# Performance work log

Measured on AMD Instinct MI355X. Metric: run time of the kernel, lower is better.

Reference implementation:

```python
import math
import jax, jax.numpy as jnp
import numpy as np

B, T_BI, D_BI = 64, 3000, 128
T_SW, D_SW = 375, 192
T_S1, D_S1 = 188, 192
N_FIRES = 300          # static fire count (target_lengths all = 300 -> beta = 1, ceil(sum)=300)
D_MODEL = 512
SCALE = 4.0            # scale_factor
EPS_LN = 1e-5


def _cif_integrate(h, alpha, thr, n_fires):
    """Vectorized CIF: cumsum + two scatter-adds (matches torch _cif_forward).
    h [B,T,D], alpha [B,T], thr [B,1] -> [B,n_fires,D]."""
    Bq, T, D = h.shape
    a = alpha / thr                       # normalize so boundaries sit at integers
    c = jnp.cumsum(a, axis=1)
    prev = c - a
    kp = jnp.floor(prev)
    kc = jnp.floor(c)
    fired = kc > kp                       # frame crosses a token boundary
    w_hi = jnp.where(fired, (c - kc) * thr, 0.0)          # leftover into new token
    w_lo = jnp.where(fired, (kp + 1.0 - prev) * thr, alpha)  # portion completing old token
    ip = jnp.clip(kp.astype(jnp.int32), 0, n_fires - 1)
    ic = jnp.clip(kc.astype(jnp.int32), 0, n_fires - 1)
    bidx = jnp.broadcast_to(jnp.arange(Bq)[:, None], (Bq, T))
    out = jnp.zeros((Bq, n_fires, D), h.dtype)
    out = out.at[bidx, ip].add(w_lo[..., None] * h)
    out = out.at[bidx, ic].add(w_hi[..., None] * h)
    return out


def _interp(src, t_cont, t_bi):
    """Linear interp of src [B,Ts,D] at continuous fire times t_cont [B,N] (given on the T_bi grid)."""
    Bq, Ts, D = src.shape
    t = t_cont * Ts / t_bi
    lo = jnp.clip(t.astype(jnp.int32), 0, Ts - 2)
    w = (t - lo.astype(t.dtype))[..., None]
    idx_lo = jnp.broadcast_to(lo[..., None], (Bq, t.shape[1], D))
    g_lo = jnp.take_along_axis(src, idx_lo, axis=1)
    g_hi = jnp.take_along_axis(src, idx_lo + 1, axis=1)
    return (1.0 - w) * g_lo + w * g_hi


def _forward(fire_signal, acoustic_src, acoustic_src_s1, conv_w, ln_g, ln_b, wp_w, wp_b,
             film_s0_w, film_s0_b, film_s1_w, film_s1_b, tproj_w, tproj_b,
             aproj_w, aproj_b, bproj_w, bproj_b, target_lengths):
    Bq, T_bi, _ = fire_signal.shape
    # 1) weight predictor: depthwise conv (k=1, no bias) -> LN -> Linear -> sigmoid
    x = fire_signal * conv_w                                   # depthwise 1x1 conv
    mu = jnp.mean(x, axis=-1, keepdims=True)
    var = jnp.var(x, axis=-1, keepdims=True)
    xn = (x - mu) * jax.lax.rsqrt(var + EPS_LN) * ln_g + ln_b
    alpha = SCALE * jax.nn.sigmoid(xn @ wp_w + wp_b)           # [B,T]
    tgt = target_lengths.astype(alpha.dtype)
    qty_loss = jnp.mean(jnp.abs(jnp.sum(alpha, axis=1) - tgt))
    # training-mode alpha normalization (sum alpha_cif == target)
    sum_a = jnp.clip(jnp.sum(alpha, axis=1, keepdims=True), 1e-8)
    alpha_cif = alpha * (tgt[:, None] / sum_a)
    # dynamic threshold beta = sum / ceil(sum)  (== 1 here since targets are integers)
    sum_cif = jnp.sum(alpha_cif, axis=1)
    ceil_sum = jax.lax.stop_gradient(jnp.clip(jnp.ceil(sum_cif), 1.0))
    thr = (sum_cif / ceil_sum)[:, None]                        # [B,1]
    # 2) CIF integration of temporal channel
    acoustic_temporal = _cif_integrate(fire_signal, alpha_cif, thr, N_FIRES)  # [B,N,128]
    # continuous fire times
    cum = jnp.cumsum(alpha_cif, axis=1)
    thresholds = jnp.arange(1, N_FIRES + 1, dtype=alpha.dtype)[None, :] * thr  # [B,N]
    ff = jax.vmap(jnp.searchsorted)(cum, thresholds)
    ff = jnp.minimum(ff, T_bi - 1)
    t_lo = jnp.maximum(ff - 1, 0)
    cum_at = jnp.take_along_axis(cum, t_lo, axis=1)
    a_at = jnp.take_along_axis(alpha_cif, ff, axis=1)
    t_cont = t_lo.astype(alpha.dtype) + (thresholds - cum_at) / jnp.clip(a_at, 1e-8)
    t_cont = jnp.clip(t_cont, 0.0, T_bi - 1)
    # 3) S0 pitch channel: interp + FiLM
    acoustic_pitch = _interp(acoustic_src, t_cont, T_bi)       # [B,N,192]
    film0 = acoustic_temporal @ film_s0_w + film_s0_b
    g0, b0 = jnp.split(film0, 2, axis=-1)
    pitch_mod = g0 * acoustic_pitch + b0
    # 4) project + combine
    embs = (acoustic_temporal @ tproj_w + tproj_b) + (pitch_mod @ aproj_w + aproj_b)
    # S1 beat channel
    acoustic_beat = _interp(acoustic_src_s1, t_cont, T_bi)     # [B,N,192]
    film1 = acoustic_temporal @ film_s1_w + film_s1_b
    g1, b1 = jnp.split(film1, 2, axis=-1)
    beat_mod = g1 * acoustic_beat + b1
    embs = embs + (beat_mod @ bproj_w + bproj_b)
    return embs, alpha, qty_loss


def setup_inputs() -> dict:
    key = jax.random.key(0)
    ks = jax.random.split(key, 14)
    # weight_proj bias init per module: alpha_init = target_fires/encoder_len
    p = min((128.0 / 3000.0) / SCALE, 0.99)
    wp_bias = math.log(p / (1.0 - p))
    f32 = jnp.float32
    return {
        "fire_signal": jax.random.normal(ks[0], (B, T_BI, D_BI), f32),
        "acoustic_src": jax.random.normal(ks[1], (B, T_SW, D_SW), f32),
        "acoustic_src_s1": jax.random.normal(ks[2], (B, T_S1, D_S1), f32),
        "target_lengths": jnp.full((B,), N_FIRES, jnp.int32),
        "conv_w": 1.0 + 0.1 * jax.random.normal(ks[3], (D_BI,), f32),
        "ln_g": jnp.ones((D_BI,), f32),
        "ln_b": jnp.zeros((D_BI,), f32),
        "wp_w": 0.02 * jax.random.normal(ks[4], (D_BI,), f32),
        "wp_b": jnp.asarray(wp_bias, f32),
        "film_s0_w": 0.02 * jax.random.normal(ks[5], (D_BI, 2 * D_SW), f32),
        "film_s0_b": jnp.concatenate([jnp.ones((D_SW,), f32), jnp.zeros((D_SW,), f32)]),
        "film_s1_w": 0.02 * jax.random.normal(ks[6], (D_BI, 2 * D_S1), f32),
        "film_s1_b": jnp.concatenate([jnp.ones((D_S1,), f32), jnp.zeros((D_S1,), f32)]),
        "tproj_w": 0.02 * jax.random.normal(ks[7], (D_BI, D_MODEL), f32),
        "tproj_b": jnp.zeros((D_MODEL,), f32),
        "aproj_w": 0.02 * jax.random.normal(ks[8], (D_SW, D_MODEL), f32),
        "aproj_b": jnp.zeros((D_MODEL,), f32),
        "bproj_w": 0.02 * jax.random.normal(ks[9], (D_S1, D_MODEL), f32),
        "bproj_b": jnp.zeros((D_MODEL,), f32),
    }


def reference(fire_signal, acoustic_src, acoustic_src_s1, target_lengths, conv_w, ln_g, ln_b,
              wp_w, wp_b, film_s0_w, film_s0_b, film_s1_w, film_s1_b, tproj_w, tproj_b,
              aproj_w, aproj_b, bproj_w, bproj_b):
    return _forward(fire_signal, acoustic_src, acoustic_src_s1, conv_w, ln_g, ln_b, wp_w, wp_b,
                    film_s0_w, film_s0_b, film_s1_w, film_s1_b, tproj_w, tproj_b,
                    aproj_w, aproj_b, bproj_w, bproj_b, target_lengths)
```

## Files before the change

kernel.cpp:

```cpp
#include <hip/hip_runtime.h>
#include <math.h>

#define BQ 64
#define TBI 3000
#define DBI 128
#define TSW 375
#define TS1 188
#define DSW 192
#define NF 300
#define DMODEL 512
#define EPSLN 1e-5f

typedef __bf16 bf16x8 __attribute__((ext_vector_type(8)));
typedef float f32x4 __attribute__((ext_vector_type(4)));

__device__ __forceinline__ unsigned short f2bf(float f) {
    unsigned u = __float_as_uint(f);
    unsigned r = (u + 0x7FFFu + ((u >> 16) & 1u)) >> 16;
    return (unsigned short)r;
}

#define ALPHA_BLOCKS 24000

__global__ __launch_bounds__(256) void k_alpha_prep(
    const float* __restrict__ fs, const float* __restrict__ conv_w,
    const float* __restrict__ ln_g, const float* __restrict__ ln_b,
    const float* __restrict__ wp_w, const float* __restrict__ wp_b,
    float* __restrict__ alpha_out,
    const float* __restrict__ f0w, const float* __restrict__ f1w,
    const float* __restrict__ tw, const float* __restrict__ aw, const float* __restrict__ bw,
    const float* __restrict__ f0b, const float* __restrict__ f1b,
    const float* __restrict__ tb, const float* __restrict__ apb, const float* __restrict__ bpb,
    unsigned short* __restrict__ Wg, unsigned short* __restrict__ Wb,
    unsigned short* __restrict__ W2,
    float* __restrict__ gbias, float* __restrict__ bbias, float* __restrict__ bias2,
    float* __restrict__ qtyo)
{
    if (blockIdx.x >= ALPHA_BLOCKS) {
        int pbid = blockIdx.x - ALPHA_BLOCKS;
        if (pbid == 1216) {
            for (int c = threadIdx.x; c < 512; c += 256) {
                if (c < 384) {
                    gbias[c] = c < 192 ? f0b[c] : f1b[c - 192];
                    bbias[c] = c < 192 ? f0b[c + 192] : f1b[c - 192 + 192];
                }
                bias2[c] = tb[c] + apb[c] + bpb[c];
            }
            if (threadIdx.x == 0) qtyo[0] = 0.f;
            return;
        }
        int i = pbid * 256 + threadIdx.x;
        if (i < 49152) {
            int j = i & 7, lane = (i >> 3) & 63, kt = (i >> 9) & 3, nt = i >> 11;
            int k = kt * 32 + (lane >> 4) * 8 + j;
            int n = nt * 16 + (lane & 15);
            float g, b;
            if (n < 192) { g = f0w[k * 384 + n];         b = f0w[k * 384 + n + 192]; }
            else         { g = f1w[k * 384 + (n - 192)]; b = f1w[k * 384 + (n - 192) + 192]; }
            Wg[i] = f2bf(g); Wb[i] = f2bf(b);
        } else {
            int ii = i - 49152;
            int j = ii & 7, lane = (ii >> 3) & 63, kt = (ii >> 9) & 15, nt = ii >> 13;
            int k = kt * 32 + (lane >> 4) * 8 + j;
            int n = nt * 16 + (lane & 15);
            float v;
            if (k < 128)      v = tw[k * 512 + n];
            else if (k < 320) v = aw[(k - 128) * 512 + n];
            else              v = bw[(k - 320) * 512 + n];
            W2[ii] = f2bf(v);
        }
        return;
    }
    int wave = threadIdx.x >> 6, lane = threadIdx.x & 63;
    int l = lane & 31;
    long g = (long)blockIdx.x * 8 + wave * 2 + (lane >> 5);
    const float* row = fs + g * DBI;
    float4 f  = *(const float4*)&row[4 * l];
    float4 cw = *(const float4*)&conv_w[4 * l];
    float4 x; x.x = f.x * cw.x; x.y = f.y * cw.y; x.z = f.z * cw.z; x.w = f.w * cw.w;
    float s = x.x + x.y + x.z + x.w;
    for (int m = 16; m >= 1; m >>= 1) s += __shfl_xor(s, m, 64);
    float mu = s * (1.0f / 128.0f);
    float4 d; d.x = x.x - mu; d.y = x.y - mu; d.z = x.z - mu; d.w = x.w - mu;
    float q = d.x * d.x + d.y * d.y + d.z * d.z + d.w * d.w;
    for (int m = 16; m >= 1; m >>= 1) q += __shfl_xor(q, m, 64);
    float var = q * (1.0f / 128.0f);
    float rs = rsqrtf(var + EPSLN);
    float4 lg = *(const float4*)&ln_g[4 * l];
    float4 lb = *(const float4*)&ln_b[4 * l];
    float4 wp = *(const float4*)&wp_w[4 * l];
    float z = (d.x * rs * lg.x + lb.x) * wp.x + (d.y * rs * lg.y + lb.y) * wp.y
            + (d.z * rs * lg.z + lb.z) * wp.z + (d.w * rs * lg.w + lb.w) * wp.w;
    for (int m = 16; m >= 1; m >>= 1) z += __shfl_xor(z, m, 64);
    z += wp_b[0];
    float a = 4.0f / (1.0f + expf(-z));
    if (l == 0) alpha_out[g] = a;
}

__global__ __launch_bounds__(1024) void k_scan3(
    const float* __restrict__ alpha, const int* __restrict__ tlen,
    float2* __restrict__ params, float* __restrict__ qtyo,
    float2* __restrict__ c2, float* __restrict__ tcont, int* __restrict__ ffout)
{
    __shared__ float2 sc[TBI];
    __shared__ float2 part[2][1024];
    __shared__ double red[1024];
    int b = blockIdx.x, tid = threadIdx.x;
    const float* ar = alpha + (long)b * TBI;
    double s = 0.0;
    for (int t = tid; t < TBI; t += 1024) s += (double)ar[t];
    red[tid] = s; __syncthreads();
    for (int d = 512; d >= 1; d >>= 1) { if (tid < d) red[tid] += red[tid + d]; __syncthreads(); }
    double sum_a = red[0]; __syncthreads();
    double tgt = (double)tlen[b];
    double sa = sum_a < 1e-8 ? 1e-8 : sum_a;
    float r = (float)(tgt / sa);
    double s2 = 0.0;
    for (int t = tid; t < TBI; t += 1024) s2 += (double)(ar[t] * r);
    red[tid] = s2; __syncthreads();
    for (int d = 512; d >= 1; d >>= 1) { if (tid < d) red[tid] += red[tid + d]; __syncthreads(); }
    float sum_cif = (float)red[0];
    float cs = ceilf(sum_cif); if (cs < 1.0f) cs = 1.0f;
    float thr = sum_cif / cs;
    float rthr = 1.0f / thr;
    if (tid == 0) {
        params[b] = make_float2(r, thr);
        atomicAdd(qtyo, (float)fabs(sum_a - tgt) * (1.0f / (float)BQ));
    }
    int base = tid * 3;
    float2 run = make_float2(0.f, 0.f);
    if (base < TBI) {
        for (int j = 0; j < 3; ++j) {
            int t = base + j;
            float ac = ar[t] * r;
            run.x += ac * rthr; run.y += ac;
            sc[t] = run;
        }
    }
    part[0][tid] = (base < TBI) ? run : make_float2(0.f, 0.f);
    __syncthreads();
    int srcb = 0;
    for (int d = 1; d < 1024; d <<= 1) {
        float2 v = part[srcb][tid];
        if (tid >= d) { float2 u = part[srcb][tid - d]; v.x += u.x; v.y += u.y; }
        part[srcb ^ 1][tid] = v;
        srcb ^= 1;
        __syncthreads();
    }
    if (base < TBI && tid > 0) {
        float2 off = part[srcb][tid - 1];
        for (int j = 0; j < 3; ++j) { sc[base + j].x += off.x; sc[base + j].y += off.y; }
    }
    __syncthreads();
    for (int t = tid; t < TBI; t += 1024) {
        float ac = ar[t] * r;
        c2[(long)b * TBI + t] = make_float2(sc[t].x, ac);
    }
    if (tid < NF) {
        float v = (float)(tid + 1) * thr;
        int lo = 0, hi = TBI;
        while (lo < hi) { int mid = (lo + hi) >> 1; if (sc[mid].y < v) lo = mid + 1; else hi = mid; }
        int ff = lo; if (ff > TBI - 1) ff = TBI - 1;
        ffout[b * NF + tid] = ff;
        int tl = ff - 1; if (tl < 0) tl = 0;
        float cum_at = sc[tl].y;
        float a_at = ar[ff] * r;
        if (a_at < 1e-8f) a_at = 1e-8f;
        float tc = (float)tl + (v - cum_at) / a_at;
        tc = fminf(fmaxf(tc, 0.0f), (float)(TBI - 1));
        tcont[b * NF + tid] = tc;
    }
}

#define TPW 3
__global__ __launch_bounds__(256) void k_cif3(
    const float* __restrict__ fs, const float2* __restrict__ c2,
    const int* __restrict__ ffA, const float2* __restrict__ params,
    unsigned short* __restrict__ at)
{
    int wid = threadIdx.x >> 6, lane = threadIdx.x & 63;
    int wg = blockIdx.x * 4 + wid;
    int b = wg / 100, slot = wg - b * 100;
    int j0 = slot * TPW;
    const int* ffb = ffA + b * NF;
    int t0 = (j0 == 0) ? 0 : ffb[j0 - 1];
    int tE = (slot == 99) ? (TBI - 1) : ffb[j0 + TPW - 1];
    float thr = params[b].y;
    float rthr = 1.0f / thr;
    const float2* cb = c2 + (long)b * TBI;
    const float* fb = fs + (long)b * TBI * DBI;
    unsigned short* ab = at + (long)b * NF * DBI;
    int nw = j0;
    int cur = -1;
    float a0 = 0.f, a1 = 0.f;
    #define FLUSH() do { \
        if (cur >= j0 && cur < j0 + TPW) { \
            while (nw < cur) { *(unsigned*)&ab[nw * DBI + 2 * lane] = 0u; ++nw; } \
            *(unsigned*)&ab[cur * DBI + 2 * lane] = (unsigned)f2bf(a0) | ((unsigned)f2bf(a1) << 16); nw = cur + 1; \
        } } while (0)
    for (int t = t0; t <= tE; ++t) {
        float2 v = cb[t];
        float2 h = *(const float2*)&fb[(long)t * DBI + 2 * lane];
        float c = v.x, ac = v.y;
        float av = ac * rthr;
        float prev = c - av;
        float kp = floorf(prev), kc = floorf(c);
        bool fired = kc > kp;
        float w_lo = fired ? (kp + 1.0f - prev) * thr : ac;
        float w_hi = fired ? (c - kc) * thr : 0.0f;
        int ip = (int)kp; if (ip > NF - 1) ip = NF - 1; if (ip < 0) ip = 0;
        int ic = (int)kc; if (ic > NF - 1) ic = NF - 1; if (ic < 0) ic = 0;
        if (ip != cur) { FLUSH(); cur = ip; a0 = 0.f; a1 = 0.f; }
        a0 += w_lo * h.x; a1 += w_lo * h.y;
        if (fired) {
            if (ic != cur) { FLUSH(); cur = ic; a0 = 0.f; a1 = 0.f; }
            a0 += w_hi * h.x; a1 += w_hi * h.y;
        }
    }
    FLUSH();
    while (nw < j0 + TPW) { *(unsigned*)&ab[nw * DBI + 2 * lane] = 0u; ++nw; }
    #undef FLUSH
}

#define EROWS 32
__global__ __launch_bounds__(512, 4) void k_emb6(
    const unsigned short* __restrict__ atb, const float* __restrict__ tcont,
    const float* __restrict__ src0, const float* __restrict__ src1,
    const unsigned short* __restrict__ Wg, const unsigned short* __restrict__ Wb,
    const unsigned short* __restrict__ W2,
    const float* __restrict__ gbias, const float* __restrict__ bbias,
    const float* __restrict__ bias2, float* __restrict__ embs)
{
    __shared__ __align__(16) unsigned short X[EROWS][520];
    __shared__ float s_w0[EROWS], s_w1[EROWS];
    __shared__ int s_lo0[EROWS], s_lo1[EROWS], s_b[EROWS];
    int tid = threadIdx.x;
    int wave = tid >> 6, lane = tid & 63;
    long r0 = (long)blockIdx.x * EROWS;
    {
        int r = tid >> 4, k8 = (tid & 15) * 8;
        *(uint4*)&X[r][k8] = *(const uint4*)&atb[(r0 + r) * DBI + k8];
    }
    if (tid < EROWS) {
        long g = r0 + tid;
        s_b[tid] = (int)(g / NF);
        float tc = tcont[g];
        float t0 = tc * ((float)TSW / 3000.0f);
        int lo0 = (int)t0; if (lo0 > TSW - 2) lo0 = TSW - 2; if (lo0 < 0) lo0 = 0;
        s_lo0[tid] = lo0; s_w0[tid] = t0 - (float)lo0;
        float t1 = tc * ((float)TS1 / 3000.0f);
        int lo1 = (int)t1; if (lo1 > TS1 - 2) lo1 = TS1 - 2; if (lo1 < 0) lo1 = 0;
        s_lo1[tid] = lo1; s_w1[tid] = t1 - (float)lo1;
    }
    __syncthreads();
    int mrow = lane & 15, quad = lane >> 4;
    for (int nt = wave; nt < 24; nt += 8) {
        f32x4 ag0 = {0,0,0,0}, ab0 = {0,0,0,0}, ag1 = {0,0,0,0}, ab1 = {0,0,0,0};
        #pragma unroll
        for (int kt = 0; kt < 4; ++kt) {
            bf16x8 a0 = *(const bf16x8*)&X[mrow][kt * 32 + quad * 8];
            bf16x8 a1 = *(const bf16x8*)&X[mrow + 16][kt * 32 + quad * 8];
            bf16x8 bg = *(const bf16x8*)&Wg[(((nt * 4 + kt) * 64) + lane) * 8];
            bf16x8 bb = *(const bf16x8*)&Wb[(((nt * 4 + kt) * 64) + lane) * 8];
            ag0 = __builtin_amdgcn_mfma_f32_16x16x32_bf16(a0, bg, ag0, 0, 0, 0);
            ab0 = __builtin_amdgcn_mfma_f32_16x16x32_bf16(a0, bb, ab0, 0, 0, 0);
            ag1 = __builtin_amdgcn_mfma_f32_16x16x32_bf16(a1, bg, ag1, 0, 0, 0);
            ab1 = __builtin_amdgcn_mfma_f32_16x16x32_bf16(a1, bb, ab1, 0, 0, 0);
        }
        int c = nt * 16 + mrow;
        bool sel = c >= DSW;
        int cc = sel ? c - DSW : c;
        const float* S = sel ? src1 : src0;
        int Ts = sel ? TS1 : TSW;
        float gb = gbias[c], bbv = bbias[c];
        #pragma unroll
        for (int q = 0; q < 4; ++q) {
            {
                int r = quad * 4 + q;
                int b = s_b[r];
                int lo = sel ? s_lo1[r] : s_lo0[r];
                float w = sel ? s_w1[r] : s_w0[r];
                const float* Sp = S + ((long)b * Ts + lo) * DSW + cc;
                float pv = (1.0f - w) * Sp[0] + w * Sp[DSW];
                X[r][128 + c] = f2bf((ag0[q] + gb) * pv + (ab0[q] + bbv));
            }
            {
                int r = quad * 4 + q + 16;
                int b = s_b[r];
                int lo = sel ? s_lo1[r] : s_lo0[r];
                float w = sel ? s_w1[r] : s_w0[r];
                const float* Sp = S + ((long)b * Ts + lo) * DSW + cc;
                float pv = (1.0f - w) * Sp[0] + w * Sp[DSW];
                X[r][128 + c] = f2bf((ag1[q] + gb) * pv + (ab1[q] + bbv));
            }
        }
    }
    __syncthreads();
    f32x4 acc[2][4];
    #pragma unroll
    for (int h = 0; h < 2; ++h)
        #pragma unroll
        for (int n = 0; n < 4; ++n) acc[h][n] = (f32x4){0, 0, 0, 0};
    for (int kt = 0; kt < 16; ++kt) {
        bf16x8 a0 = *(const bf16x8*)&X[mrow][kt * 32 + quad * 8];
        bf16x8 a1 = *(const bf16x8*)&X[mrow + 16][kt * 32 + quad * 8];
        #pragma unroll
        for (int n = 0; n < 4; ++n) {
            int nt = wave * 4 + n;
            bf16x8 bfv = *(const bf16x8*)&W2[((nt * 16 + kt) * 64 + lane) * 8];
            acc[0][n] = __builtin_amdgcn_mfma_f32_16x16x32_bf16(a0, bfv, acc[0][n], 0, 0, 0);
            acc[1][n] = __builtin_amdgcn_mfma_f32_16x16x32_bf16(a1, bfv, acc[1][n], 0, 0, 0);
        }
    }
    #pragma unroll
    for (int n = 0; n < 4; ++n) {
        int cbase = (wave * 4 + n) * 16 + mrow;
        float bv = bias2[cbase];
        #pragma unroll
        for (int q = 0; q < 4; ++q) {
            embs[(r0 + quad * 4 + q) * DMODEL + cbase] = acc[0][n][q] + bv;
            embs[(r0 + 16 + quad * 4 + q) * DMODEL + cbase] = acc[1][n][q] + bv;
        }
    }
}

extern "C" void kernel_launch(void* const* d_in, const int* in_sizes, int n_in,
                              void* d_out, int out_size, void* d_ws, size_t ws_size,
                              hipStream_t stream)
{
    const float* fs     = (const float*)d_in[0];
    const float* src0   = (const float*)d_in[1];
    const float* src1   = (const float*)d_in[2];
    const int*   tlen   = (const int*)d_in[3];
    const float* conv_w = (const float*)d_in[4];
    const float* ln_g   = (const float*)d_in[5];
    const float* ln_b   = (const float*)d_in[6];
    const float* wp_w   = (const float*)d_in[7];
    const float* wp_b   = (const float*)d_in[8];
    const float* f0w    = (const float*)d_in[9];
    const float* f0b    = (const float*)d_in[10];
    const float* f1w    = (const float*)d_in[11];
    const float* f1b    = (const float*)d_in[12];
    const float* tw     = (const float*)d_in[13];
    const float* tb     = (const float*)d_in[14];
    const float* aw     = (const float*)d_in[15];
    const float* apb    = (const float*)d_in[16];
    const float* bw     = (const float*)d_in[17];
    const float* bpb    = (const float*)d_in[18];

    float* embs  = (float*)d_out;
    float* alpha = embs + (long)BQ * NF * DMODEL;
    float* qtyo  = alpha + (long)BQ * TBI;

    char* ws = (char*)d_ws;
    size_t off = 0;
    unsigned short* at = (unsigned short*)(ws + off); off += 4915200;
    float2* c2     = (float2*)(ws + off); off += 1536000;
    float*  tcont  = (float*)(ws + off);  off += 76800;
    int*    ffA    = (int*)(ws + off);    off += 76800;
    float2* params = (float2*)(ws + off); off += 512;
    unsigned short* Wg = (unsigned short*)(ws + off); off += 98304;
    unsigned short* Wb = (unsigned short*)(ws + off); off += 98304;
    unsigned short* W2 = (unsigned short*)(ws + off); off += 524288;
    float* gbias = (float*)(ws + off); off += 1536;
    float* bbias = (float*)(ws + off); off += 1536;
    float* bias2 = (float*)(ws + off); off += 2048;

    k_alpha_prep<<<ALPHA_BLOCKS + 1217, 256, 0, stream>>>(
        fs, conv_w, ln_g, ln_b, wp_w, wp_b, alpha,
        f0w, f1w, tw, aw, bw, f0b, f1b, tb, apb, bpb,
        Wg, Wb, W2, gbias, bbias, bias2, qtyo);
    k_scan3<<<BQ, 1024, 0, stream>>>(alpha, tlen, params, qtyo, c2, tcont, ffA);
    k_cif3<<<(BQ * 100) / 4, 256, 0, stream>>>(fs, c2, ffA, params, at);
    k_emb6<<<(BQ * NF) / EROWS, 512, 0, stream>>>(at, tcont, src0, src1,
                                                  Wg, Wb, W2, gbias, bbias, bias2, embs);
}
```

Measured before the change: 265.4 us.

## Use wave-shuffle reductions, one wave per fire in CIF, 64-row embedding tiles

The scan kernel replaces its shared-memory tree reductions, which needed many barriers, with wave shuffle reductions followed by a small cross-wave step. The CIF kernel now assigns one wave per output fire instead of three, which removes the flush/zero-fill bookkeeping and triples the wave count, at the cost of re-reading boundary frames. The embedding kernel processes 64 rows per block instead of 32, so each loaded weight fragment feeds four MFMAs, but it holds more accumulators and launches half as many blocks. The EROWS-sized shared arrays and the interpolation buffers grow accordingly.

```diff
diff --git a/kernel.cpp b/kernel.cpp
--- a/kernel.cpp
+++ b/kernel.cpp
@@ -97,29 +97,45 @@
     if (l == 0) alpha_out[g] = a;
 }
 
-__global__ __launch_bounds__(1024) void k_scan3(
+__global__ __launch_bounds__(1024) void k_scan4(
     const float* __restrict__ alpha, const int* __restrict__ tlen,
     float2* __restrict__ params, float* __restrict__ qtyo,
     float2* __restrict__ c2, float* __restrict__ tcont, int* __restrict__ ffout)
 {
     __shared__ float2 sc[TBI];
     __shared__ float2 part[2][1024];
-    __shared__ double red[1024];
+    __shared__ double wpart[16];
     int b = blockIdx.x, tid = threadIdx.x;
+    int wv = tid >> 6, ln = tid & 63;
     const float* ar = alpha + (long)b * TBI;
     double s = 0.0;
     for (int t = tid; t < TBI; t += 1024) s += (double)ar[t];
-    red[tid] = s; __syncthreads();
-    for (int d = 512; d >= 1; d >>= 1) { if (tid < d) red[tid] += red[tid + d]; __syncthreads(); }
-    double sum_a = red[0]; __syncthreads();
+    for (int m = 32; m >= 1; m >>= 1) s += __shfl_xor(s, m, 64);
+    if (ln == 0) wpart[wv] = s;
+    __syncthreads();
+    if (wv == 0) {
+        double d = (ln < 16) ? wpart[ln] : 0.0;
+        for (int m = 8; m >= 1; m >>= 1) d += __shfl_xor(d, m, 64);
+        if (ln == 0) wpart[0] = d;
+    }
+    __syncthreads();
+    double sum_a = wpart[0];
+    __syncthreads();
     double tgt = (double)tlen[b];
     double sa = sum_a < 1e-8 ? 1e-8 : sum_a;
     float r = (float)(tgt / sa);
     double s2 = 0.0;
     for (int t = tid; t < TBI; t += 1024) s2 += (double)(ar[t] * r);
-    red[tid] = s2; __syncthreads();
-    for (int d = 512; d >= 1; d >>= 1) { if (tid < d) red[tid] += red[tid + d]; __syncthreads(); }
-    float sum_cif = (float)red[0];
+    for (int m = 32; m >= 1; m >>= 1) s2 += __shfl_xor(s2, m, 64);
+    if (ln == 0) wpart[wv] = s2;
+    __syncthreads();
+    if (wv == 0) {
+        double d = (ln < 16) ? wpart[ln] : 0.0;
+        for (int m = 8; m >= 1; m >>= 1) d += __shfl_xor(d, m, 64);
+        if (ln == 0) wpart[0] = d;
+    }
+    __syncthreads();
+    float sum_cif = (float)wpart[0];
     float cs = ceilf(sum_cif); if (cs < 1.0f) cs = 1.0f;
     float thr = sum_cif / cs;
     float rthr = 1.0f / thr;
@@ -172,33 +188,23 @@
     }
 }
 
-#define TPW 3
-__global__ __launch_bounds__(256) void k_cif3(
+__global__ __launch_bounds__(256) void k_cif4(
     const float* __restrict__ fs, const float2* __restrict__ c2,
     const int* __restrict__ ffA, const float2* __restrict__ params,
     unsigned short* __restrict__ at)
 {
     int wid = threadIdx.x >> 6, lane = threadIdx.x & 63;
     int wg = blockIdx.x * 4 + wid;
-    int b = wg / 100, slot = wg - b * 100;
-    int j0 = slot * TPW;
+    int b = wg / NF, j = wg - b * NF;
     const int* ffb = ffA + b * NF;
-    int t0 = (j0 == 0) ? 0 : ffb[j0 - 1];
-    int tE = (slot == 99) ? (TBI - 1) : ffb[j0 + TPW - 1];
+    int s = (j == 0) ? 0 : ffb[j - 1];
+    int e = (j == NF - 1) ? (TBI - 1) : ffb[j];
     float thr = params[b].y;
     float rthr = 1.0f / thr;
     const float2* cb = c2 + (long)b * TBI;
     const float* fb = fs + (long)b * TBI * DBI;
-    unsigned short* ab = at + (long)b * NF * DBI;
-    int nw = j0;
-    int cur = -1;
     float a0 = 0.f, a1 = 0.f;
-    #define FLUSH() do { \
-        if (cur >= j0 && cur < j0 + TPW) { \
-            while (nw < cur) { *(unsigned*)&ab[nw * DBI + 2 * lane] = 0u; ++nw; } \
-            *(unsigned*)&ab[cur * DBI + 2 * lane] = (unsigned)f2bf(a0) | ((unsigned)f2bf(a1) << 16); nw = cur + 1; \
-        } } while (0)
-    for (int t = t0; t <= tE; ++t) {
+    for (int t = s; t <= e; ++t) {
         float2 v = cb[t];
         float2 h = *(const float2*)&fb[(long)t * DBI + 2 * lane];
         float c = v.x, ac = v.y;
@@ -210,20 +216,15 @@
         float w_hi = fired ? (c - kc) * thr : 0.0f;
         int ip = (int)kp; if (ip > NF - 1) ip = NF - 1; if (ip < 0) ip = 0;
         int ic = (int)kc; if (ic > NF - 1) ic = NF - 1; if (ic < 0) ic = 0;
-        if (ip != cur) { FLUSH(); cur = ip; a0 = 0.f; a1 = 0.f; }
-        a0 += w_lo * h.x; a1 += w_lo * h.y;
-        if (fired) {
-            if (ic != cur) { FLUSH(); cur = ic; a0 = 0.f; a1 = 0.f; }
-            a0 += w_hi * h.x; a1 += w_hi * h.y;
-        }
-    }
-    FLUSH();
-    while (nw < j0 + TPW) { *(unsigned*)&ab[nw * DBI + 2 * lane] = 0u; ++nw; }
-    #undef FLUSH
-}
-
-#define EROWS 32
-__global__ __launch_bounds__(512, 4) void k_emb6(
+        if (ip == j) { a0 += w_lo * h.x; a1 += w_lo * h.y; }
+        if (fired && ic == j) { a0 += w_hi * h.x; a1 += w_hi * h.y; }
+    }
+    unsigned short* ab = at + (long)b * NF * DBI;
+    *(unsigned*)&ab[j * DBI + 2 * lane] = (unsigned)f2bf(a0) | ((unsigned)f2bf(a1) << 16);
+}
+
+#define EROWS 64
+__global__ __launch_bounds__(512, 4) void k_emb7(
     const unsigned short* __restrict__ atb, const float* __restrict__ tcont,
     const float* __restrict__ src0, const float* __restrict__ src1,
     const unsigned short* __restrict__ Wg, const unsigned short* __restrict__ Wb,
@@ -237,8 +238,8 @@
     int tid = threadIdx.x;
     int wave = tid >> 6, lane = tid & 63;
     long r0 = (long)blockIdx.x * EROWS;
-    {
-        int r = tid >> 4, k8 = (tid & 15) * 8;
+    for (int idx = tid; idx < 1024; idx += 512) {
+        int r = idx >> 4, k8 = (idx & 15) * 8;
         *(uint4*)&X[r][k8] = *(const uint4*)&atb[(r0 + r) * DBI + k8];
     }
     if (tid < EROWS) {
@@ -255,17 +256,19 @@
     __syncthreads();
     int mrow = lane & 15, quad = lane >> 4;
     for (int nt = wave; nt < 24; nt += 8) {
-        f32x4 ag0 = {0,0,0,0}, ab0 = {0,0,0,0}, ag1 = {0,0,0,0}, ab1 = {0,0,0,0};
+        f32x4 ag[4], av[4];
+        #pragma unroll
+        for (int m = 0; m < 4; ++m) { ag[m] = (f32x4){0,0,0,0}; av[m] = (f32x4){0,0,0,0}; }
         #pragma unroll
         for (int kt = 0; kt < 4; ++kt) {
-            bf16x8 a0 = *(const bf16x8*)&X[mrow][kt * 32 + quad * 8];
-            bf16x8 a1 = *(const bf16x8*)&X[mrow + 16][kt * 32 + quad * 8];
             bf16x8 bg = *(const bf16x8*)&Wg[(((nt * 4 + kt) * 64) + lane) * 8];
             bf16x8 bb = *(const bf16x8*)&Wb[(((nt * 4 + kt) * 64) + lane) * 8];
-            ag0 = __builtin_amdgcn_mfma_f32_16x16x32_bf16(a0, bg, ag0, 0, 0, 0);
-            ab0 = __builtin_amdgcn_mfma_f32_16x16x32_bf16(a0, bb, ab0, 0, 0, 0);
-            ag1 = __builtin_amdgcn_mfma_f32_16x16x32_bf16(a1, bg, ag1, 0, 0, 0);
-            ab1 = __builtin_amdgcn_mfma_f32_16x16x32_bf16(a1, bb, ab1, 0, 0, 0);
+            #pragma unroll
+            for (int m = 0; m < 4; ++m) {
+                bf16x8 a = *(const bf16x8*)&X[mrow + 16 * m][kt * 32 + quad * 8];
+                ag[m] = __builtin_amdgcn_mfma_f32_16x16x32_bf16(a, bg, ag[m], 0, 0, 0);
+                av[m] = __builtin_amdgcn_mfma_f32_16x16x32_bf16(a, bb, av[m], 0, 0, 0);
+            }
         }
         int c = nt * 16 + mrow;
         bool sel = c >= DSW;
@@ -274,42 +277,36 @@
         int Ts = sel ? TS1 : TSW;
         float gb = gbias[c], bbv = bbias[c];
         #pragma unroll
-        for (int q = 0; q < 4; ++q) {
-            {
-                int r = quad * 4 + q;
+        for (int m = 0; m < 4; ++m) {
+            #pragma unroll
+            for (int q = 0; q < 4; ++q) {
+                int r = 16 * m + quad * 4 + q;
                 int b = s_b[r];
                 int lo = sel ? s_lo1[r] : s_lo0[r];
                 float w = sel ? s_w1[r] : s_w0[r];
                 const float* Sp = S + ((long)b * Ts + lo) * DSW + cc;
                 float pv = (1.0f - w) * Sp[0] + w * Sp[DSW];
-                X[r][128 + c] = f2bf((ag0[q] + gb) * pv + (ab0[q] + bbv));
+                X[r][128 + c] = f2bf((ag[m][q] + gb) * pv + (av[m][q] + bbv));
             }
-            {
-                int r = quad * 4 + q + 16;
-                int b = s_b[r];
-                int lo = sel ? s_lo1[r] : s_lo0[r];
-                float w = sel ? s_w1[r] : s_w0[r];
-                const float* Sp = S + ((long)b * Ts + lo) * DSW + cc;
-                float pv = (1.0f - w) * Sp[0] + w * Sp[DSW];
-                X[r][128 + c] = f2bf((ag1[q] + gb) * pv + (ab1[q] + bbv));
-            }
-        }
-    }
-    __syncthreads();
-    f32x4 acc[2][4];
+        }
+    }
+    __syncthreads();
+    f32x4 acc[4][4];
     #pragma unroll
-    for (int h = 0; h < 2; ++h)
-        #pragma unroll
-        for (int n = 0; n < 4; ++n) acc[h][n] = (f32x4){0, 0, 0, 0};
+    for (int m = 0; m < 4; ++m)
+        #pragma unroll
+        for (int n = 0; n < 4; ++n) acc[m][n] = (f32x4){0, 0, 0, 0};
     for (int kt = 0; kt < 16; ++kt) {
-        bf16x8 a0 = *(const bf16x8*)&X[mrow][kt * 32 + quad * 8];
-        bf16x8 a1 = *(const bf16x8*)&X[mrow + 16][kt * 32 + quad * 8];
+        bf16x8 a[4];
+        #pragma unroll
+        for (int m = 0; m < 4; ++m) a[m] = *(const bf16x8*)&X[mrow + 16 * m][kt * 32 + quad * 8];
         #pragma unroll
         for (int n = 0; n < 4; ++n) {
             int nt = wave * 4 + n;
             bf16x8 bfv = *(const bf16x8*)&W2[((nt * 16 + kt) * 64 + lane) * 8];
-            acc[0][n] = __builtin_amdgcn_mfma_f32_16x16x32_bf16(a0, bfv, acc[0][n], 0, 0, 0);
-            acc[1][n] = __builtin_amdgcn_mfma_f32_16x16x32_bf16(a1, bfv, acc[1][n], 0, 0, 0);
+            #pragma unroll
+            for (int m = 0; m < 4; ++m)
+                acc[m][n] = __builtin_amdgcn_mfma_f32_16x16x32_bf16(a[m], bfv, acc[m][n], 0, 0, 0);
         }
     }
     #pragma unroll
@@ -317,10 +314,10 @@
         int cbase = (wave * 4 + n) * 16 + mrow;
         float bv = bias2[cbase];
         #pragma unroll
-        for (int q = 0; q < 4; ++q) {
-            embs[(r0 + quad * 4 + q) * DMODEL + cbase] = acc[0][n][q] + bv;
-            embs[(r0 + 16 + quad * 4 + q) * DMODEL + cbase] = acc[1][n][q] + bv;
-        }
+        for (int m = 0; m < 4; ++m)
+            #pragma unroll
+            for (int q = 0; q < 4; ++q)
+                embs[(r0 + 16 * m + quad * 4 + q) * DMODEL + cbase] = acc[m][n][q] + bv;
     }
 }
 
@@ -370,8 +367,8 @@
         fs, conv_w, ln_g, ln_b, wp_w, wp_b, alpha,
         f0w, f1w, tw, aw, bw, f0b, f1b, tb, apb, bpb,
         Wg, Wb, W2, gbias, bbias, bias2, qtyo);
-    k_scan3<<<BQ, 1024, 0, stream>>>(alpha, tlen, params, qtyo, c2, tcont, ffA);
-    k_cif3<<<(BQ * 100) / 4, 256, 0, stream>>>(fs, c2, ffA, params, at);
-    k_emb6<<<(BQ * NF) / EROWS, 512, 0, stream>>>(at, tcont, src0, src1,
+    k_scan4<<<BQ, 1024, 0, stream>>>(alpha, tlen, params, qtyo, c2, tcont, ffA);
+    k_cif4<<<(BQ * NF) / 4, 256, 0, stream>>>(fs, c2, ffA, params, at);
+    k_emb7<<<(BQ * NF) / EROWS, 512, 0, stream>>>(at, tcont, src0, src1,
                                                   Wg, Wb, W2, gbias, bbias, bias2, embs);
 }
```

After: 286.0 us. 1.08x slower.
